# Optimization experiments

Measured on AMD Instinct MI355X. Metric: run time of the kernel, lower is better.

The kernel has to match this reference:

```python
import jax, jax.numpy as jnp
import numpy as np

N_NODES = 50000
N_EDGES = 800000
N_GRAPHS = 64
NEG_SLOPE = 0.2  # PyG GATConv default LeakyReLU slope


def _gat_layer(x, src, dst, W, a_src, a_dst, bias, n_nodes):
    """Single-head GATConv: gather -> segment-softmax over dst -> scatter-add."""
    h = x @ W                                   # [N, F]
    e = jax.nn.leaky_relu(
        (h @ a_src)[src] + (h @ a_dst)[dst], NEG_SLOPE)  # [E]
    # numerically-stable segment softmax over incoming edges of each dst node
    m = jax.ops.segment_max(e, dst, num_segments=n_nodes)   # [N]
    e = jnp.exp(e - m[dst])
    s = jax.ops.segment_sum(e, dst, num_segments=n_nodes)   # [N]
    alpha = e / s[dst]                                       # [E]
    out = jax.ops.segment_sum(alpha[:, None] * h[src], dst, num_segments=n_nodes)
    return out + bias


def setup_inputs() -> dict:
    key = jax.random.key(0)
    ks = jax.random.split(key, 16)
    x = jax.random.normal(ks[0], (N_NODES, 3), dtype=jnp.float32)
    edge_index = jax.random.randint(ks[1], (2, N_EDGES), 0, N_NODES, dtype=jnp.int64)
    edge_attr = jax.random.normal(ks[2], (N_EDGES, 4), dtype=jnp.float32)
    batch = jnp.sort(jax.random.randint(ks[3], (N_NODES,), 0, N_GRAPHS, dtype=jnp.int64))

    def glorot(k, shape):
        lim = float(np.sqrt(6.0 / (shape[0] + shape[-1])))
        return jax.random.uniform(k, shape, jnp.float32, -lim, lim)

    return {
        "x": x, "edge_index": edge_index, "edge_attr": edge_attr, "batch": batch,
        "W1": glorot(ks[4], (3, 8)),
        "a_src1": glorot(ks[5], (8,)),
        "a_dst1": glorot(ks[6], (8,)),
        "b1": jnp.zeros((8,), jnp.float32),
        "W2": glorot(ks[7], (8, 256)),
        "a_src2": glorot(ks[8], (256,)),
        "a_dst2": glorot(ks[9], (256,)),
        "b2": jnp.zeros((256,), jnp.float32),
        "fc_w": glorot(ks[10], (256, 1)),
        "fc_b": jnp.zeros((1,), jnp.float32),
    }


def reference(x, edge_index, edge_attr, batch,
              W1, a_src1, a_dst1, b1, W2, a_src2, a_dst2, b2, fc_w, fc_b):
    n = x.shape[0]
    loops = jnp.arange(n, dtype=edge_index.dtype)
    src = jnp.concatenate([edge_index[0], loops])  # add_self_loops=True
    dst = jnp.concatenate([edge_index[1], loops])
    # edge_attr is unused by GATConv when edge_dim=None (PyG default)
    h = jax.nn.relu(_gat_layer(x, src, dst, W1, a_src1, a_dst1, b1, n))
    h = jax.nn.relu(_gat_layer(h, src, dst, W2, a_src2, a_dst2, b2, n))
    h = h @ fc_w + fc_b                               # [N, 1]
    out = jax.ops.segment_sum(h, batch, num_segments=N_GRAPHS)  # global_add_pool
    return out
```

## Files before the change

kernel.cpp:

```cpp
#include <hip/hip_runtime.h>
#include <math.h>

static constexpr int NN = 50000;
static constexpr int NE = 800000;
static constexpr int NG = 64;
static constexpr int CAP = 64;
static constexpr float SLOPE = 0.2f;
static constexpr int WDER_BLK = 3125;

__global__ void __launch_bounds__(256) k_init_all(
    const float* __restrict__ x, const float* __restrict__ W1,
    const float* __restrict__ a1s, const float* __restrict__ a1d,
    const int* __restrict__ ei,
    const float* __restrict__ W2, const float* __restrict__ a2s,
    const float* __restrict__ a2d,
    float* __restrict__ h1, float* __restrict__ hs1, float* __restrict__ hd1,
    int* __restrict__ counts, int* __restrict__ ell,
    float* __restrict__ w2sd, float* __restrict__ out) {
  if (blockIdx.x == WDER_BLK) {
    if (threadIdx.x < NG) out[threadIdx.x] = 0.f;
    int w = threadIdx.x >> 6, lane = threadIdx.x & 63;
    for (int tt = w * 4; tt < w * 4 + 4; ++tt) {
      int k = tt >> 1, sel = tt & 1;
      const float* a = sel ? a2d : a2s;
      float acc = 0.f;
      for (int j = lane; j < 256; j += 64) acc += W2[256 * k + j] * a[j];
      for (int off = 32; off; off >>= 1) acc += __shfl_down(acc, off);
      if (lane == 0) w2sd[tt] = acc;
    }
    return;
  }
  int t = blockIdx.x * 256 + threadIdx.x;
  if (t < NN) {
    float x0 = x[3*t], x1 = x[3*t+1], x2 = x[3*t+2];
    float hs = 0.f, hd = 0.f;
    float v[8];
#pragma unroll
    for (int f = 0; f < 8; ++f) {
      v[f] = x0 * W1[f] + x1 * W1[8+f] + x2 * W1[16+f];
      hs += v[f] * a1s[f];
      hd += v[f] * a1d[f];
    }
    float4* h4 = reinterpret_cast<float4*>(h1 + 8*t);
    h4[0] = make_float4(v[0], v[1], v[2], v[3]);
    h4[1] = make_float4(v[4], v[5], v[6], v[7]);
    hs1[t] = hs; hd1[t] = hd;
  }
  if (t < NE) {
    int s = ei[t];
    int d = ei[NE + t];
    int r = atomicAdd(&counts[d], 1);
    if (r < CAP) ell[d * CAP + r] = s;
  }
}

__device__ __forceinline__ void gather16(int n, int l, int deg,
                                         const int* __restrict__ row,
                                         const float* __restrict__ hs,
                                         const float* __restrict__ hd,
                                         const float* __restrict__ feat,
                                         float acc[8]) {
  float hdn = hd[n];
  float s = 0.f;
#pragma unroll
  for (int f = 0; f < 8; ++f) acc[f] = 0.f;
  for (int j = l - 1; j < deg; j += 16) {
    int src = (j < 0) ? n : row[j];
    float el = hs[src] + hdn;
    el = el >= 0.f ? el : SLOPE * el;
    float w = __expf(el);
    s += w;
    const float4* f4 = reinterpret_cast<const float4*>(feat + 8*src);
    float4 lo = f4[0], hi = f4[1];
    acc[0] += w*lo.x; acc[1] += w*lo.y; acc[2] += w*lo.z; acc[3] += w*lo.w;
    acc[4] += w*hi.x; acc[5] += w*hi.y; acc[6] += w*hi.z; acc[7] += w*hi.w;
  }
#pragma unroll
  for (int off = 8; off; off >>= 1) {
    s += __shfl_xor(s, off, 16);
#pragma unroll
    for (int f = 0; f < 8; ++f) acc[f] += __shfl_xor(acc[f], off, 16);
  }
  float inv = 1.f / s;
#pragma unroll
  for (int f = 0; f < 8; ++f) acc[f] *= inv;
}

__global__ void __launch_bounds__(256) k_layer1(
    const int* __restrict__ counts, const int* __restrict__ ell,
    const float* __restrict__ h1, const float* __restrict__ hs1,
    const float* __restrict__ hd1, const float* __restrict__ b1,
    const float* __restrict__ w2sd,
    float* __restrict__ out1, float* __restrict__ hs2, float* __restrict__ hd2) {
  int t = blockIdx.x * 256 + threadIdx.x;
  int n = t >> 4, l = t & 15;
  if (n >= NN) return;
  int deg = min(counts[n], CAP);
  float acc[8];
  gather16(n, l, deg, ell + n * CAP, hs1, hd1, h1, acc);
  if (l == 0) {
    float hs = 0.f, hd = 0.f;
    float v[8];
#pragma unroll
    for (int f = 0; f < 8; ++f) {
      v[f] = fmaxf(acc[f] + b1[f], 0.f);
      hs += v[f] * w2sd[2*f];
      hd += v[f] * w2sd[2*f+1];
    }
    float4* o4 = reinterpret_cast<float4*>(out1 + 8*n);
    o4[0] = make_float4(v[0], v[1], v[2], v[3]);
    o4[1] = make_float4(v[4], v[5], v[6], v[7]);
    hs2[n] = hs; hd2[n] = hd;
  }
}

__global__ void __launch_bounds__(256) k_layer2final(
    const int* __restrict__ counts, const int* __restrict__ ell,
    const float* __restrict__ out1, const float* __restrict__ hs2,
    const float* __restrict__ hd2, const float* __restrict__ b2,
    const float* __restrict__ W2, const float* __restrict__ fcw,
    const float* __restrict__ fcb, const int* __restrict__ batch,
    float* __restrict__ out) {
  __shared__ float sW2[2048];
  __shared__ float sb2[256];
  __shared__ float sfc[256];
  __shared__ float bins[NG];
  for (int i = threadIdx.x; i < 2048; i += 256) sW2[i] = W2[i];
  sb2[threadIdx.x] = b2[threadIdx.x];
  sfc[threadIdx.x] = fcw[threadIdx.x];
  if (threadIdx.x < NG) bins[threadIdx.x] = 0.f;
  __syncthreads();

  int t = blockIdx.x * 256 + threadIdx.x;
  int n = t >> 4, l = t & 15;
  if (n < NN) {
    int deg = min(counts[n], CAP);
    float acc[8];
    gather16(n, l, deg, ell + n * CAP, hs2, hd2, out1, acc);
    float y = 0.f;
    for (int i = 0; i < 16; ++i) {
      int j = l + 16 * i;
      float o = sb2[j];
#pragma unroll
      for (int k = 0; k < 8; ++k) o += acc[k] * sW2[256*k + j];
      o = fmaxf(o, 0.f);
      y += o * sfc[j];
    }
#pragma unroll
    for (int off = 8; off; off >>= 1) y += __shfl_xor(y, off, 16);
    if (l == 0) atomicAdd(&bins[batch[n]], y + fcb[0]);
  }
  __syncthreads();
  if (threadIdx.x < NG) {
    float v = bins[threadIdx.x];
    if (v != 0.f) atomicAdd(&out[threadIdx.x], v);
  }
}

extern "C" void kernel_launch(void* const* d_in, const int* in_sizes, int n_in,
                              void* d_out, int out_size, void* d_ws, size_t ws_size,
                              hipStream_t stream) {
  const float* x    = (const float*)d_in[0];
  const int*   ei   = (const int*)d_in[1];
  const int*   batch= (const int*)d_in[3];
  const float* W1   = (const float*)d_in[4];
  const float* a1s  = (const float*)d_in[5];
  const float* a1d  = (const float*)d_in[6];
  const float* b1   = (const float*)d_in[7];
  const float* W2   = (const float*)d_in[8];
  const float* a2s  = (const float*)d_in[9];
  const float* a2d  = (const float*)d_in[10];
  const float* b2   = (const float*)d_in[11];
  const float* fcw  = (const float*)d_in[12];
  const float* fcb  = (const float*)d_in[13];
  float* out = (float*)d_out;

  float* ws   = (float*)d_ws;
  float* h1   = ws;
  float* out1 = h1   + 400000;
  float* hs1  = out1 + 400000;
  float* hd1  = hs1  + 50000;
  float* hs2  = hd1  + 50000;
  float* hd2  = hs2  + 50000;
  float* w2sd = hd2  + 50000;
  int* counts = (int*)(w2sd + 16);
  int* ell    = counts + 50000;

  hipMemsetAsync(counts, 0, NN * sizeof(int), stream);

  k_init_all<<<3126, 256, 0, stream>>>(x, W1, a1s, a1d, ei, W2, a2s, a2d,
                                       h1, hs1, hd1, counts, ell, w2sd, out);
  k_layer1<<<3125, 256, 0, stream>>>(counts, ell, h1, hs1, hd1, b1, w2sd,
                                     out1, hs2, hd2);
  k_layer2final<<<3125, 256, 0, stream>>>(counts, ell, out1, hs2, hd2, b2,
                                          W2, fcw, fcb, batch, out);
}
```

Baseline: 185.9 us.

## Build ELL adjacency with per-block shared-memory counters instead of global atomics

Replaces the global-atomic ELL construction with 128 blocks, each owning a contiguous range of destination nodes. Each block scans the whole destination array and uses shared-memory atomics for its own nodes, then writes clamped counts, which removes the memset and the per-use clamps. This avoids contended global atomics, but every block now re-reads the full edge list, and only 128 blocks are launched.

```diff
diff --git a/kernel.cpp b/kernel.cpp
--- a/kernel.cpp
+++ b/kernel.cpp
@@ -6,9 +6,10 @@
 static constexpr int NG = 64;
 static constexpr int CAP = 64;
 static constexpr float SLOPE = 0.2f;
-static constexpr int WDER_BLK = 3125;
-
-__global__ void __launch_bounds__(256) k_init_all(
+static constexpr int NB = 128;
+static constexpr int DPB = (NN + NB - 1) / NB;
+
+__global__ void __launch_bounds__(256) k_build(
     const float* __restrict__ x, const float* __restrict__ W1,
     const float* __restrict__ a1s, const float* __restrict__ a1d,
     const int* __restrict__ ei,
@@ -17,7 +18,12 @@
     float* __restrict__ h1, float* __restrict__ hs1, float* __restrict__ hd1,
     int* __restrict__ counts, int* __restrict__ ell,
     float* __restrict__ w2sd, float* __restrict__ out) {
-  if (blockIdx.x == WDER_BLK) {
+  __shared__ int lcnt[DPB];
+  int base = blockIdx.x * DPB;
+  int lim = min(base + DPB, NN);
+  for (int i = threadIdx.x; i < DPB; i += 256) lcnt[i] = 0;
+
+  if (blockIdx.x == 0) {
     if (threadIdx.x < NG) out[threadIdx.x] = 0.f;
     int w = threadIdx.x >> 6, lane = threadIdx.x & 63;
     for (int tt = w * 4; tt < w * 4 + 4; ++tt) {
@@ -28,11 +34,11 @@
       for (int off = 32; off; off >>= 1) acc += __shfl_down(acc, off);
       if (lane == 0) w2sd[tt] = acc;
     }
-    return;
-  }
-  int t = blockIdx.x * 256 + threadIdx.x;
-  if (t < NN) {
-    float x0 = x[3*t], x1 = x[3*t+1], x2 = x[3*t+2];
+  }
+  __syncthreads();
+
+  for (int n = base + threadIdx.x; n < lim; n += 256) {
+    float x0 = x[3*n], x1 = x[3*n+1], x2 = x[3*n+2];
     float hs = 0.f, hd = 0.f;
     float v[8];
 #pragma unroll
@@ -41,16 +47,25 @@
       hs += v[f] * a1s[f];
       hd += v[f] * a1d[f];
     }
-    float4* h4 = reinterpret_cast<float4*>(h1 + 8*t);
+    float4* h4 = reinterpret_cast<float4*>(h1 + 8*n);
     h4[0] = make_float4(v[0], v[1], v[2], v[3]);
     h4[1] = make_float4(v[4], v[5], v[6], v[7]);
-    hs1[t] = hs; hd1[t] = hd;
-  }
-  if (t < NE) {
-    int s = ei[t];
-    int d = ei[NE + t];
-    int r = atomicAdd(&counts[d], 1);
-    if (r < CAP) ell[d * CAP + r] = s;
+    hs1[n] = hs; hd1[n] = hd;
+  }
+
+  const int4* dst4 = reinterpret_cast<const int4*>(ei + NE);
+  for (int i = threadIdx.x; i < NE/4; i += 256) {
+    int4 d = dst4[i];
+    int e = 4*i;
+    if (d.x >= base && d.x < lim) { int r = atomicAdd(&lcnt[d.x-base],1); if (r<CAP) ell[d.x*CAP+r] = ei[e];   }
+    if (d.y >= base && d.y < lim) { int r = atomicAdd(&lcnt[d.y-base],1); if (r<CAP) ell[d.y*CAP+r] = ei[e+1]; }
+    if (d.z >= base && d.z < lim) { int r = atomicAdd(&lcnt[d.z-base],1); if (r<CAP) ell[d.z*CAP+r] = ei[e+2]; }
+    if (d.w >= base && d.w < lim) { int r = atomicAdd(&lcnt[d.w-base],1); if (r<CAP) ell[d.w*CAP+r] = ei[e+3]; }
+  }
+  __syncthreads();
+  for (int i = threadIdx.x; i < DPB; i += 256) {
+    int n = base + i;
+    if (n < lim) counts[n] = min(lcnt[i], CAP);
   }
 }
 
@@ -95,7 +110,7 @@
   int t = blockIdx.x * 256 + threadIdx.x;
   int n = t >> 4, l = t & 15;
   if (n >= NN) return;
-  int deg = min(counts[n], CAP);
+  int deg = counts[n];
   float acc[8];
   gather16(n, l, deg, ell + n * CAP, hs1, hd1, h1, acc);
   if (l == 0) {
@@ -134,7 +149,7 @@
   int t = blockIdx.x * 256 + threadIdx.x;
   int n = t >> 4, l = t & 15;
   if (n < NN) {
-    int deg = min(counts[n], CAP);
+    int deg = counts[n];
     float acc[8];
     gather16(n, l, deg, ell + n * CAP, hs2, hd2, out1, acc);
     float y = 0.f;
@@ -186,10 +201,8 @@
   int* counts = (int*)(w2sd + 16);
   int* ell    = counts + 50000;
 
-  hipMemsetAsync(counts, 0, NN * sizeof(int), stream);
-
-  k_init_all<<<3126, 256, 0, stream>>>(x, W1, a1s, a1d, ei, W2, a2s, a2d,
-                                       h1, hs1, hd1, counts, ell, w2sd, out);
+  k_build<<<NB, 256, 0, stream>>>(x, W1, a1s, a1d, ei, W2, a2s, a2d,
+                                  h1, hs1, hd1, counts, ell, w2sd, out);
   k_layer1<<<3125, 256, 0, stream>>>(counts, ell, h1, hs1, hd1, b1, w2sd,
                                      out1, hs2, hd2);
   k_layer2final<<<3125, 256, 0, stream>>>(counts, ell, out1, hs2, hd2, b2,
```

After: 592.3 us. 3.19x slower.
